# Performance work log

Hardware: AMD Instinct MI355X
Metric: run time of the kernel (lower is better)

## Reference

```python
import jax, jax.numpy as jnp
import numpy as np

B, L, D = 4, 2048, 1024

def setup_inputs() -> dict:
    key = jax.random.key(0)
    k = jax.random.split(key, 5)
    s = 1.0 / np.sqrt(D)
    return {
        "x": jax.random.normal(k[0], (B, L, D), dtype=jnp.float32),
        "W1": jax.random.uniform(k[1], (D, D), jnp.float32, -s, s),
        "b1": jax.random.uniform(k[2], (D,), jnp.float32, -s, s),
        "W2": jax.random.uniform(k[3], (D, D), jnp.float32, -s, s),
        "b2": jax.random.uniform(k[4], (D,), jnp.float32, -s, s),
    }

def reference(x, W1, b1, W2, b2):
    # query = fc1(x), value = fc2(x); torch Linear: x @ W^T + b
    query = jnp.einsum("bld,ed->ble", x, W1) + b1   # [B,L,D]
    value = jnp.einsum("bld,ed->ble", x, W2) + b2   # [B,L,D]
    # attn = softmax(query @ value^T)  (dot attention, no scaling in original)
    scores = jnp.einsum("bqd,bkd->bqk", query, value)  # [B,L,L]
    attn = jax.nn.softmax(scores, axis=-1)
    # dropout_p=0.0 -> identity
    return jnp.einsum("bqk,bkd->bqd", attn, value)     # [B,L,D]
```

## Files before the change

### kernel.cpp

```cpp
#include <hip/hip_runtime.h>
#include <stdint.h>
#include <stddef.h>


typedef _Float16  f16_t;
typedef _Float16  f16x8 __attribute__((ext_vector_type(8)));
typedef float     f32x4 __attribute__((ext_vector_type(4)));

__device__ __forceinline__ f32x4 mfma16(f16x8 a, f16x8 b, f32x4 c) {
  return __builtin_amdgcn_mfma_f32_16x16x32_f16(a, b, c, 0, 0, 0);
}

__device__ __forceinline__ void async_copy16(const f16_t* g, f16_t* l) {
  __builtin_amdgcn_global_load_lds(
      (const __attribute__((address_space(1))) unsigned int*)(g),
      (__attribute__((address_space(3))) unsigned int*)(l),
      16, 0, 0);
}

template <int RM, int RN, int NS>
__device__ __forceinline__ void gemm_core(
    const f16_t* __restrict__ A, const f16_t* __restrict__ B,
    int lda, int ldb, int nk,
    f16_t* __restrict__ As, f16_t* __restrict__ Bs, f32x4 (&acc)[RM][RN])
{
  const int tid  = threadIdx.x;
  const int lane = tid & 63;
  const int w    = tid >> 6;
  const int wr   = (w >> 1) * (RM * 16);
  const int wc   = (w & 1) * (RN * 16);
  const int l16  = lane & 15;
  const int quad = lane >> 4;
  const int sw   = (quad ^ ((l16 >> 1) & 3)) * 8;

  const int r0  = tid >> 2;
  const int kc0 = ((tid & 3) ^ ((r0 >> 1) & 3)) * 8;

  const f16_t* Ag = A + (size_t)r0 * lda + kc0;
  const f16_t* Bg = B + (size_t)r0 * ldb + kc0;

  for (int kt = 0; kt < nk; ++kt) {
#pragma unroll
    for (int s = 0; s < NS; ++s) {
      const int ko = s * 32;
#pragma unroll
      for (int h = 0; h < RM / 2; ++h)
        async_copy16(Ag + ko + (size_t)(64 * h) * lda,
                     As + s * RM * 1024 + (tid + 256 * h) * 8);
#pragma unroll
      for (int h = 0; h < RN / 2; ++h)
        async_copy16(Bg + ko + (size_t)(64 * h) * ldb,
                     Bs + s * RN * 1024 + (tid + 256 * h) * 8);
    }
    __syncthreads();

#pragma unroll
    for (int s = 0; s < NS; ++s) {
      const f16_t* Ac = As + s * RM * 1024;
      const f16_t* Bc = Bs + s * RN * 1024;
      f16x8 af[RM], bf[RN];
#pragma unroll
      for (int i = 0; i < RM; ++i)
        af[i] = *(const f16x8*)(Ac + (wr + i * 16 + l16) * 32 + sw);
#pragma unroll
      for (int j = 0; j < RN; ++j)
        bf[j] = *(const f16x8*)(Bc + (wc + j * 16 + l16) * 32 + sw);
#pragma unroll
      for (int i = 0; i < RM; ++i)
#pragma unroll
        for (int j = 0; j < RN; ++j)
          acc[i][j] = mfma16(af[i], bf[j], acc[i][j]);
    }

    __syncthreads();
    Ag += NS * 32; Bg += NS * 32;
  }
}

__global__ __launch_bounds__(256) void cvt_kernel(
    const float* __restrict__ x, const float* __restrict__ W1,
    const float* __restrict__ W2, f16_t* __restrict__ xh,
    f16_t* __restrict__ W1h, f16_t* __restrict__ W2h)
{
  const size_t XN = (size_t)8192 * 1024;
  const size_t WN = (size_t)1024 * 1024;
  size_t i = ((size_t)blockIdx.x * 256 + threadIdx.x) * 8;
  const float* in; f16_t* out;
  if (i < XN)            { in = x;  out = xh; }
  else if (i < XN + WN)  { in = W1; out = W1h; i -= XN; }
  else                   { in = W2; out = W2h; i -= XN + WN; }
  f32x4 a = *(const f32x4*)(in + i);
  f32x4 b = *(const f32x4*)(in + i + 4);
  f16x8 o;
#pragma unroll
  for (int k = 0; k < 4; ++k) { o[k] = (f16_t)a[k]; o[k + 4] = (f16_t)b[k]; }
  *(f16x8*)(out + i) = o;
}

__global__ __launch_bounds__(256) void proj_qv_kernel(
    const f16_t* __restrict__ X, const f16_t* __restrict__ W1,
    const f16_t* __restrict__ W2, const float* __restrict__ b1,
    const float* __restrict__ b2, f16_t* __restrict__ Q,
    f16_t* __restrict__ V, f16_t* __restrict__ Vt)
{
  __shared__ __align__(16) f16_t Xs[2 * 64 * 32];
  __shared__ __align__(16) f16_t W1s[2 * 64 * 32];
  __shared__ __align__(16) f16_t W2s[2 * 64 * 32];
  constexpr int SZ = 64 * 32;

  const int m0 = blockIdx.x * 64;
  const int n0 = blockIdx.y * 64;

  const int tid  = threadIdx.x;
  const int lane = tid & 63;
  const int w    = tid >> 6;
  const int wr   = (w >> 1) * 32;
  const int wc   = (w & 1) * 32;
  const int quad = lane >> 4;
  const int l16  = lane & 15;
  const int sw   = (quad ^ ((l16 >> 1) & 3)) * 8;
  const int r0   = tid >> 2;
  const int kc0  = ((tid & 3) ^ ((r0 >> 1) & 3)) * 8;

  const f16_t* Xg = X + (size_t)(m0 + r0) * 1024 + kc0;
  const f16_t* G1 = W1 + (size_t)(n0 + r0) * 1024 + kc0;
  const f16_t* G2 = W2 + (size_t)(n0 + r0) * 1024 + kc0;

  f32x4 accQ[2][2] = {};
  f32x4 accV[2][2] = {};

  for (int kt = 0; kt < 16; ++kt) {
#pragma unroll
    for (int s = 0; s < 2; ++s) {
      const int ko = s * 32;
      async_copy16(Xg + ko, Xs + s * SZ + tid * 8);
      async_copy16(G1 + ko, W1s + s * SZ + tid * 8);
      async_copy16(G2 + ko, W2s + s * SZ + tid * 8);
    }
    __syncthreads();

#pragma unroll
    for (int s = 0; s < 2; ++s) {
      f16x8 xf[2], w1f[2], w2f[2];
#pragma unroll
      for (int i = 0; i < 2; ++i) {
        xf[i]  = *(const f16x8*)(Xs  + s * SZ + (wr + i * 16 + l16) * 32 + sw);
        w1f[i] = *(const f16x8*)(W1s + s * SZ + (wc + i * 16 + l16) * 32 + sw);
        w2f[i] = *(const f16x8*)(W2s + s * SZ + (wc + i * 16 + l16) * 32 + sw);
      }
#pragma unroll
      for (int i = 0; i < 2; ++i)
#pragma unroll
        for (int j = 0; j < 2; ++j) {
          accQ[i][j] = mfma16(xf[i], w1f[j], accQ[i][j]);
          accV[i][j] = mfma16(xf[i], w2f[j], accV[i][j]);
        }
    }
    __syncthreads();
    Xg += 64; G1 += 64; G2 += 64;
  }

  f16_t* Ts = W1s;
#pragma unroll
  for (int j = 0; j < 2; ++j) {
    const int c   = wc + j * 16 + l16;
    const int col = n0 + c;
    const float bq = b1[col], bv = b2[col];
#pragma unroll
    for (int i = 0; i < 2; ++i)
#pragma unroll
      for (int r = 0; r < 4; ++r) {
        const int k   = wr + i * 16 + quad * 4 + r;
        const int row = m0 + k;
        const float q = accQ[i][j][r] + bq;
        const float v = accV[i][j][r] + bv;
        Q[(size_t)row * 1024 + col] = (f16_t)q;
        V[(size_t)row * 1024 + col] = (f16_t)v;
        Ts[c * 64 + (((k >> 3) ^ (c >> 3)) << 3) + (k & 7)] = (f16_t)v;
      }
  }
  __syncthreads();

  const size_t vtbase = ((size_t)(m0 >> 11) << 21) + (size_t)n0 * 2048 + (m0 & 2047);
#pragma unroll
  for (int rep = 0; rep < 2; ++rep) {
    const int d = rep * 32 + (tid >> 3);
    const int c = tid & 7;
    f16x8 vv = *(const f16x8*)(Ts + d * 64 + ((c ^ (d >> 3)) << 3));
    *(f16x8*)(Vt + vtbase + (size_t)d * 2048 + c * 8) = vv;
  }
}

__global__ __launch_bounds__(256) void score_kernel(
    const f16_t* __restrict__ Q, const f16_t* __restrict__ V,
    f16_t* __restrict__ S)
{
  __shared__ __align__(16) f16_t As[2 * 128 * 32];
  __shared__ __align__(16) f16_t Bs[2 * 128 * 32];
  const int m0 = blockIdx.x * 128;
  const int n0 = blockIdx.y * 128;
  const size_t boff = (size_t)blockIdx.z * 2048 * 1024;

  f32x4 acc[4][4] = {};
  gemm_core<4, 4, 2>(Q + boff + (size_t)m0 * 1024,
                     V + boff + (size_t)n0 * 1024,
                     1024, 1024, 1024 / 64, As, Bs, acc);

  f16_t* Sb = S + (size_t)blockIdx.z * 2048 * 2048;
  const int lane = threadIdx.x & 63;
  const int w    = threadIdx.x >> 6;
  const int wr   = (w >> 1) * 64, wc = (w & 1) * 64;
  const int quad = lane >> 4,     l16 = lane & 15;

#pragma unroll
  for (int i = 0; i < 4; ++i)
#pragma unroll
    for (int j = 0; j < 4; ++j)
#pragma unroll
      for (int r = 0; r < 4; ++r) {
        const int row = m0 + wr + i * 16 + quad * 4 + r;
        const int col = n0 + wc + j * 16 + l16;
        Sb[(size_t)row * 2048 + col] = (f16_t)acc[i][j][r];
      }
}

__global__ __launch_bounds__(256) void softmax_kernel(f16_t* __restrict__ S)
{
  f16_t* row = S + (size_t)blockIdx.x * 2048;
  const int tid  = threadIdx.x;
  const int lane = tid & 63;
  const int w    = tid >> 6;

  f16x8 v = *((const f16x8*)row + tid);
  float f[8];
#pragma unroll
  for (int k = 0; k < 8; ++k) f[k] = (float)v[k];

  float m = f[0];
#pragma unroll
  for (int k = 1; k < 8; ++k) m = fmaxf(m, f[k]);
#pragma unroll
  for (int off = 32; off >= 1; off >>= 1) m = fmaxf(m, __shfl_xor(m, off));

  __shared__ float red[4];
  if (lane == 0) red[w] = m;
  __syncthreads();
  m = fmaxf(fmaxf(red[0], red[1]), fmaxf(red[2], red[3]));

  float s = 0.f;
#pragma unroll
  for (int k = 0; k < 8; ++k) { f[k] = __expf(f[k] - m); s += f[k]; }
#pragma unroll
  for (int off = 32; off >= 1; off >>= 1) s += __shfl_xor(s, off);
  __syncthreads();
  if (lane == 0) red[w] = s;
  __syncthreads();
  s = (red[0] + red[1]) + (red[2] + red[3]);
  const float inv = 1.f / s;

  f16x8 o;
#pragma unroll
  for (int k = 0; k < 8; ++k) o[k] = (f16_t)(f[k] * inv);
  *((f16x8*)row + tid) = o;
}

__global__ __launch_bounds__(256) void out_kernel(
    const f16_t* __restrict__ P, const f16_t* __restrict__ Vt,
    float* __restrict__ Out)
{
  __shared__ __align__(16) f16_t As[2 * 64 * 32];
  __shared__ __align__(16) f16_t Bs[2 * 128 * 32];
  const int m0 = blockIdx.x * 64;
  const int n0 = blockIdx.y * 128;
  const size_t poff  = (size_t)blockIdx.z * 2048 * 2048;
  const size_t vtoff = (size_t)blockIdx.z * 1024 * 2048;

  f32x4 acc[2][4] = {};
  gemm_core<2, 4, 2>(P + poff + (size_t)m0 * 2048,
                     Vt + vtoff + (size_t)n0 * 2048,
                     2048, 2048, 2048 / 64, As, Bs, acc);

  float* Ob = Out + (size_t)blockIdx.z * 2048 * 1024;
  const int lane = threadIdx.x & 63;
  const int w    = threadIdx.x >> 6;
  const int wr   = (w >> 1) * 32, wc = (w & 1) * 64;
  const int quad = lane >> 4,     l16 = lane & 15;

#pragma unroll
  for (int i = 0; i < 2; ++i)
#pragma unroll
    for (int j = 0; j < 4; ++j)
#pragma unroll
      for (int r = 0; r < 4; ++r) {
        const int row = m0 + wr + i * 16 + quad * 4 + r;
        const int col = n0 + wc + j * 16 + l16;
        Ob[(size_t)row * 1024 + col] = acc[i][j][r];
      }
}

extern "C" void kernel_launch(void* const* d_in, const int* in_sizes, int n_in,
                              void* d_out, int out_size, void* d_ws, size_t ws_size,
                              hipStream_t stream) {
  const float* x  = (const float*)d_in[0];
  const float* W1 = (const float*)d_in[1];
  const float* b1 = (const float*)d_in[2];
  const float* W2 = (const float*)d_in[3];
  const float* b2 = (const float*)d_in[4];
  float* out = (float*)d_out;

  const size_t QN = (size_t)8192 * 1024;
  const size_t WN = (size_t)1024 * 1024;
  f16_t* xh  = (f16_t*)d_ws;
  f16_t* W1h = xh + QN;
  f16_t* W2h = W1h + WN;
  f16_t* Q   = W2h + WN;
  f16_t* V   = Q + QN;
  f16_t* Vt  = V + QN;
  f16_t* S   = Vt + QN;

  dim3 blk(256);
  cvt_kernel<<<5120, blk, 0, stream>>>(x, W1, W2, xh, W1h, W2h);
  proj_qv_kernel<<<dim3(128, 16), blk, 0, stream>>>(xh, W1h, W2h, b1, b2, Q, V, Vt);
  score_kernel<<<dim3(16, 16, 4), blk, 0, stream>>>(Q, V, S);
  softmax_kernel<<<8192, blk, 0, stream>>>(S);
  out_kernel<<<dim3(32, 8, 4), blk, 0, stream>>>(S, Vt, out);
}
```

Measured before the change: 251.2 us.

## Double-buffer LDS tiles with async prefetch of next K-slice in GEMMs

```diff
diff --git a/kernel.cpp b/kernel.cpp
--- a/kernel.cpp
+++ b/kernel.cpp
@@ -18,7 +18,11 @@
       16, 0, 0);
 }
 
-template <int RM, int RN, int NS>
+#define WAIT_VM(N) asm volatile("s_waitcnt vmcnt(" #N ")" ::: "memory")
+#define WAIT_LGKM0() asm volatile("s_waitcnt lgkmcnt(0)" ::: "memory")
+#define BARRIER() asm volatile("s_barrier" ::: "memory")
+
+template <int RM, int RN>
 __device__ __forceinline__ void gemm_core(
     const f16_t* __restrict__ A, const f16_t* __restrict__ B,
     int lda, int ldb, int nk,
@@ -39,41 +43,57 @@
   const f16_t* Ag = A + (size_t)r0 * lda + kc0;
   const f16_t* Bg = B + (size_t)r0 * ldb + kc0;
 
+  constexpr int ASZ = RM * 1024;
+  constexpr int BSZ = RN * 1024;
+  constexpr int NP  = RM / 2 + RN / 2;
+
+#pragma unroll
+  for (int h = 0; h < RM / 2; ++h)
+    async_copy16(Ag + (size_t)(64 * h) * lda, As + (tid + 256 * h) * 8);
+#pragma unroll
+  for (int h = 0; h < RN / 2; ++h)
+    async_copy16(Bg + (size_t)(64 * h) * ldb, Bs + (tid + 256 * h) * 8);
+  Ag += 32; Bg += 32;
+
+  int cur = 0;
   for (int kt = 0; kt < nk; ++kt) {
-#pragma unroll
-    for (int s = 0; s < NS; ++s) {
-      const int ko = s * 32;
+    if (kt + 1 < nk) {
+      const int nxt = cur ^ 1;
 #pragma unroll
       for (int h = 0; h < RM / 2; ++h)
-        async_copy16(Ag + ko + (size_t)(64 * h) * lda,
-                     As + s * RM * 1024 + (tid + 256 * h) * 8);
+        async_copy16(Ag + (size_t)(64 * h) * lda,
+                     As + nxt * ASZ + (tid + 256 * h) * 8);
 #pragma unroll
       for (int h = 0; h < RN / 2; ++h)
-        async_copy16(Bg + ko + (size_t)(64 * h) * ldb,
-                     Bs + s * RN * 1024 + (tid + 256 * h) * 8);
+        async_copy16(Bg + (size_t)(64 * h) * ldb,
+                     Bs + nxt * BSZ + (tid + 256 * h) * 8);
+      Ag += 32; Bg += 32;
+      if constexpr (NP == 3)      WAIT_VM(3);
+      else if constexpr (NP == 4) WAIT_VM(4);
+      else                        WAIT_VM(0);
+    } else {
+      WAIT_VM(0);
     }
-    __syncthreads();
-
-#pragma unroll
-    for (int s = 0; s < NS; ++s) {
-      const f16_t* Ac = As + s * RM * 1024;
-      const f16_t* Bc = Bs + s * RN * 1024;
-      f16x8 af[RM], bf[RN];
-#pragma unroll
-      for (int i = 0; i < RM; ++i)
-        af[i] = *(const f16x8*)(Ac + (wr + i * 16 + l16) * 32 + sw);
+    BARRIER();
+
+    const f16_t* Ac = As + cur * ASZ;
+    const f16_t* Bc = Bs + cur * BSZ;
+    f16x8 af[RM], bf[RN];
+#pragma unroll
+    for (int i = 0; i < RM; ++i)
+      af[i] = *(const f16x8*)(Ac + (wr + i * 16 + l16) * 32 + sw);
+#pragma unroll
+    for (int j = 0; j < RN; ++j)
+      bf[j] = *(const f16x8*)(Bc + (wc + j * 16 + l16) * 32 + sw);
+#pragma unroll
+    for (int i = 0; i < RM; ++i)
 #pragma unroll
       for (int j = 0; j < RN; ++j)
-        bf[j] = *(const f16x8*)(Bc + (wc + j * 16 + l16) * 32 + sw);
-#pragma unroll
-      for (int i = 0; i < RM; ++i)
-#pragma unroll
-        for (int j = 0; j < RN; ++j)
-          acc[i][j] = mfma16(af[i], bf[j], acc[i][j]);
-    }
-
-    __syncthreads();
-    Ag += NS * 32; Bg += NS * 32;
+        acc[i][j] = mfma16(af[i], bf[j], acc[i][j]);
+
+    WAIT_LGKM0();
+    BARRIER();
+    cur ^= 1;
   }
 }
 
@@ -129,35 +149,44 @@
   f32x4 accQ[2][2] = {};
   f32x4 accV[2][2] = {};
 
-  for (int kt = 0; kt < 16; ++kt) {
-#pragma unroll
-    for (int s = 0; s < 2; ++s) {
-      const int ko = s * 32;
-      async_copy16(Xg + ko, Xs + s * SZ + tid * 8);
-      async_copy16(G1 + ko, W1s + s * SZ + tid * 8);
-      async_copy16(G2 + ko, W2s + s * SZ + tid * 8);
+  async_copy16(Xg, Xs + tid * 8);
+  async_copy16(G1, W1s + tid * 8);
+  async_copy16(G2, W2s + tid * 8);
+  Xg += 32; G1 += 32; G2 += 32;
+
+  int cur = 0;
+  for (int kt = 0; kt < 32; ++kt) {
+    if (kt + 1 < 32) {
+      const int nxt = cur ^ 1;
+      async_copy16(Xg, Xs + nxt * SZ + tid * 8);
+      async_copy16(G1, W1s + nxt * SZ + tid * 8);
+      async_copy16(G2, W2s + nxt * SZ + tid * 8);
+      Xg += 32; G1 += 32; G2 += 32;
+      WAIT_VM(3);
+    } else {
+      WAIT_VM(0);
     }
-    __syncthreads();
-
-#pragma unroll
-    for (int s = 0; s < 2; ++s) {
-      f16x8 xf[2], w1f[2], w2f[2];
-#pragma unroll
-      for (int i = 0; i < 2; ++i) {
-        xf[i]  = *(const f16x8*)(Xs  + s * SZ + (wr + i * 16 + l16) * 32 + sw);
-        w1f[i] = *(const f16x8*)(W1s + s * SZ + (wc + i * 16 + l16) * 32 + sw);
-        w2f[i] = *(const f16x8*)(W2s + s * SZ + (wc + i * 16 + l16) * 32 + sw);
+    BARRIER();
+
+    const int o = cur * SZ;
+    f16x8 xf[2], w1f[2], w2f[2];
+#pragma unroll
+    for (int i = 0; i < 2; ++i) {
+      xf[i]  = *(const f16x8*)(Xs  + o + (wr + i * 16 + l16) * 32 + sw);
+      w1f[i] = *(const f16x8*)(W1s + o + (wc + i * 16 + l16) * 32 + sw);
+      w2f[i] = *(const f16x8*)(W2s + o + (wc + i * 16 + l16) * 32 + sw);
+    }
+#pragma unroll
+    for (int i = 0; i < 2; ++i)
+#pragma unroll
+      for (int j = 0; j < 2; ++j) {
+        accQ[i][j] = mfma16(xf[i], w1f[j], accQ[i][j]);
+        accV[i][j] = mfma16(xf[i], w2f[j], accV[i][j]);
       }
-#pragma unroll
-      for (int i = 0; i < 2; ++i)
-#pragma unroll
-        for (int j = 0; j < 2; ++j) {
-          accQ[i][j] = mfma16(xf[i], w1f[j], accQ[i][j]);
-          accV[i][j] = mfma16(xf[i], w2f[j], accV[i][j]);
-        }
-    }
-    __syncthreads();
-    Xg += 64; G1 += 64; G2 += 64;
+
+    WAIT_LGKM0();
+    BARRIER();
+    cur ^= 1;
   }
 
   f16_t* Ts = W1s;
@@ -202,9 +231,9 @@
   const size_t boff = (size_t)blockIdx.z * 2048 * 1024;
 
   f32x4 acc[4][4] = {};
-  gemm_core<4, 4, 2>(Q + boff + (size_t)m0 * 1024,
-                     V + boff + (size_t)n0 * 1024,
-                     1024, 1024, 1024 / 64, As, Bs, acc);
+  gemm_core<4, 4>(Q + boff + (size_t)m0 * 1024,
+                  V + boff + (size_t)n0 * 1024,
+                  1024, 1024, 1024 / 32, As, Bs, acc);
 
   f16_t* Sb = S + (size_t)blockIdx.z * 2048 * 2048;
   const int lane = threadIdx.x & 63;
@@ -276,9 +305,9 @@
   const size_t vtoff = (size_t)blockIdx.z * 1024 * 2048;
 
   f32x4 acc[2][4] = {};
-  gemm_core<2, 4, 2>(P + poff + (size_t)m0 * 2048,
-                     Vt + vtoff + (size_t)n0 * 2048,
-                     2048, 2048, 2048 / 64, As, Bs, acc);
+  gemm_core<2, 4>(P + poff + (size_t)m0 * 2048,
+                  Vt + vtoff + (size_t)n0 * 2048,
+                  2048, 2048, 2048 / 32, As, Bs, acc);
 
   float* Ob = Out + (size_t)blockIdx.z * 2048 * 1024;
   const int lane = threadIdx.x & 63;
```

Measured after the change: 279.1 us. +11.1%, slower.
